# Kernel optimization log

Hardware: AMD Instinct MI355X
Metric: run time of the kernel (lower is better)

The kernel has to match this reference:

```python
import jax, jax.numpy as jnp
import numpy as np


def setup_inputs() -> dict:
    key = jax.random.key(0)
    k1, k2, k3, k4 = jax.random.split(key, 4)
    b, c, h, w = 16, 1024, 32, 32
    dim = h * w  # 1024
    x = jax.random.normal(k1, (b, c, h, w), dtype=jnp.float32)
    cond_img = jax.random.normal(k2, (b, c, h, w), dtype=jnp.float32)
    # torch nn.Linear weights: (out_features, in_features), y = x @ W.T
    Wq = jax.random.normal(k3, (dim, dim), dtype=jnp.float32) * (dim ** -0.5)
    Wkv = jax.random.normal(k4, (2 * dim, dim), dtype=jnp.float32) * (dim ** -0.5)
    return {"x": x, "cond_img": cond_img, "Wq": Wq, "Wkv": Wkv}


def reference(x, cond_img, Wq, Wkv):
    b, c, h, w = x.shape
    dim = h * w
    scale = dim ** -0.5
    xf = x.reshape(b, c, dim)          # (b, c, dim)
    cf = cond_img.reshape(b, c, dim)   # (b, c, dim)
    q = jnp.einsum('bcd,od->bco', xf, Wq)          # (b, c, dim)
    kv = jnp.einsum('bcd,od->bco', cf, Wkv)        # (b, c, 2*dim)
    k, v = jnp.split(kv, 2, axis=-1)               # each (b, c, dim)
    attn = jnp.einsum('bic,bjc->bij', q, k) * scale  # (b, c, c)
    attn = jax.nn.softmax(attn, axis=-1)
    out = jnp.einsum('bij,bjc->bic', attn, v)      # (b, c, dim)
    return out.reshape(b, c, h, w)
```

## Files before the change

### kernel.cpp

```cpp
#include <hip/hip_runtime.h>
#include <stdint.h>


typedef __bf16 bf16_t;
typedef bf16_t bf16x8 __attribute__((ext_vector_type(8)));
typedef float f32x4 __attribute__((ext_vector_type(4)));

#define AS1 __attribute__((address_space(1)))
#define AS3 __attribute__((address_space(3)))

__device__ __forceinline__ uint16_t f2bf(float f) {
  bf16_t h = (bf16_t)f;
  return __builtin_bit_cast(uint16_t, h);
}

__global__ __launch_bounds__(256) void cvt_all(
    const float* __restrict__ x, const float* __restrict__ c,
    const float* __restrict__ wq, const float* __restrict__ wkv,
    uint16_t* __restrict__ XB, uint16_t* __restrict__ CB,
    uint16_t* __restrict__ WQB, uint16_t* __restrict__ WKVB) {
  long i = (long)blockIdx.x * 256 + threadIdx.x;
  if (i >= 9175040) return;
  const float* src;
  uint16_t* dst;
  long off;
  if (i < 4194304) { src = x; dst = XB; off = i; }
  else if (i < 8388608) { src = c; dst = CB; off = i - 4194304; }
  else if (i < 8650752) { src = wq; dst = WQB; off = i - 8388608; }
  else { src = wkv; dst = WKVB; off = i - 8650752; }
  float4 v = ((const float4*)src)[off];
  ushort4 o;
  o.x = f2bf(v.x); o.y = f2bf(v.y); o.z = f2bf(v.z); o.w = f2bf(v.w);
  ((ushort4*)dst)[off] = o;
}

__device__ __forceinline__ void stage_tile(const uint16_t* __restrict__ g,
                                           int ldK, uint16_t* lds, int tid) {
#pragma unroll
  for (int i = 0; i < 4; ++i) {
    int cix = i * 512 + tid;
    int row = cix >> 3;
    int ch = cix & 7;
    int sch = ch ^ (row & 7);
    const uint16_t* gp = g + row * ldK + sch * 8;
    __builtin_amdgcn_global_load_lds((AS1 void*)gp,
                                     (AS3 void*)((uint8_t*)lds + cix * 16), 16,
                                     0, 0);
  }
}

template <int MODE>
__global__ __launch_bounds__(512, 2) void gemm_bt(
    const uint16_t* __restrict__ A, const uint16_t* __restrict__ B,
    void* __restrict__ C0, void* __restrict__ C1, int K, int N,
    long long sA, long long sB, long long sC, float scale) {
  __shared__ uint16_t smem[65536];

  const int tid = threadIdx.x;
  const int lane = tid & 63;
  const int wid = tid >> 6;
  const int wr = wid >> 2;
  const int wc = wid & 3;
  const int lr = lane & 15, lg = lane >> 4;
  const int ch0 = lr & 7;

  const int gx = gridDim.x, gy = gridDim.y;
  const int nwg = gx * gy * gridDim.z;
  int fid = blockIdx.x + gx * (blockIdx.y + gy * blockIdx.z);
  int swz = (fid & 7) * (nwg >> 3) + (fid >> 3);
  const int bx = swz % gx;
  const int rem = swz / gx;
  const int by = rem % gy;
  const int bz = rem / gy;

  const int row0 = by * 256;
  const int col0 = bx * 256;
  const uint16_t* At = A + (long long)bz * sA + (long long)row0 * K;
  const uint16_t* Bt = B + (long long)bz * sB + (long long)col0 * K;

  const int NT = K >> 6;

  stage_tile(At, K, smem, tid);
  stage_tile(Bt, K, smem + 32768, tid);
  stage_tile(At + 64, K, smem + 16384, tid);
  stage_tile(Bt + 64, K, smem + 49152, tid);
  asm volatile("s_waitcnt vmcnt(8)" ::: "memory");
  __builtin_amdgcn_s_barrier();

  f32x4 acc[8][4] = {};
  bf16x8 aA_[4][2];
  bf16x8 aB_[4][2];
  bf16x8 bF[4][2];

  {
    const uint8_t* sa = (const uint8_t*)smem;
#pragma unroll
    for (int mi = 0; mi < 4; ++mi)
#pragma unroll
      for (int kk = 0; kk < 2; ++kk)
        aA_[mi][kk] = *(const bf16x8*)(sa + (wr * 128 + mi * 16 + lr) * 128 +
                                       (((kk * 4 + lg) ^ ch0) << 4));
  }

  for (int t = 0; t < NT; ++t) {
    const uint8_t* sa = (const uint8_t*)(smem + (t & 1) * 16384);
    const uint8_t* sb = (const uint8_t*)(smem + 32768 + (t & 1) * 16384);

#pragma unroll
    for (int nj = 0; nj < 4; ++nj)
#pragma unroll
      for (int kk = 0; kk < 2; ++kk)
        bF[nj][kk] =
            *(const bf16x8*)(sb + (wc * 64 + nj * 16 + lr) * 128 +
                             (((kk * 4 + lg) ^ ch0) << 4));
#pragma unroll
    for (int mi = 0; mi < 4; ++mi)
#pragma unroll
      for (int kk = 0; kk < 2; ++kk)
        aB_[mi][kk] =
            *(const bf16x8*)(sa + (wr * 128 + 64 + mi * 16 + lr) * 128 +
                             (((kk * 4 + lg) ^ ch0) << 4));
    __builtin_amdgcn_s_setprio(1);
#pragma unroll
    for (int kk = 0; kk < 2; ++kk)
#pragma unroll
      for (int mi = 0; mi < 4; ++mi)
#pragma unroll
        for (int nj = 0; nj < 4; ++nj)
          acc[mi][nj] = __builtin_amdgcn_mfma_f32_16x16x32_bf16(
              aA_[mi][kk], bF[nj][kk], acc[mi][nj], 0, 0, 0);
    __builtin_amdgcn_s_setprio(0);
    if (t + 1 < NT) asm volatile("s_waitcnt vmcnt(4)" ::: "memory");
    asm volatile("s_waitcnt lgkmcnt(0)" ::: "memory");
    __builtin_amdgcn_s_barrier();

    if (t + 2 < NT) {
      stage_tile(At + (t + 2) * 64, K, smem + (t & 1) * 16384, tid);
      stage_tile(Bt + (t + 2) * 64, K, smem + 32768 + (t & 1) * 16384, tid);
    }
    if (t + 1 < NT) {
      const uint8_t* sa2 = (const uint8_t*)(smem + ((t + 1) & 1) * 16384);
#pragma unroll
      for (int mi = 0; mi < 4; ++mi)
#pragma unroll
        for (int kk = 0; kk < 2; ++kk)
          aA_[mi][kk] =
              *(const bf16x8*)(sa2 + (wr * 128 + mi * 16 + lr) * 128 +
                               (((kk * 4 + lg) ^ ch0) << 4));
    }
    __builtin_amdgcn_s_setprio(1);
#pragma unroll
    for (int kk = 0; kk < 2; ++kk)
#pragma unroll
      for (int mi = 0; mi < 4; ++mi)
#pragma unroll
        for (int nj = 0; nj < 4; ++nj)
          acc[4 + mi][nj] = __builtin_amdgcn_mfma_f32_16x16x32_bf16(
              aB_[mi][kk], bF[nj][kk], acc[4 + mi][nj], 0, 0, 0);
    __builtin_amdgcn_s_setprio(0);
    if (t + 2 < NT)
      asm volatile("s_waitcnt vmcnt(8)" ::: "memory");
    else
      asm volatile("s_waitcnt vmcnt(0)" ::: "memory");
    __builtin_amdgcn_s_barrier();
  }

  if (MODE == 1 && col0 >= 1024) {
    __syncthreads();
#pragma unroll
    for (int mi = 0; mi < 8; ++mi) {
#pragma unroll
      for (int ni = 0; ni < 4; ++ni) {
        const int cc = wc * 64 + ni * 16 + lr;
        const int jjb = wr * 128 + mi * 16 + lg * 4;
        ushort4 o;
        o.x = f2bf(acc[mi][ni][0]);
        o.y = f2bf(acc[mi][ni][1]);
        o.z = f2bf(acc[mi][ni][2]);
        o.w = f2bf(acc[mi][ni][3]);
        *(ushort4*)&smem[cc * 256 + (jjb ^ ((cc & 7) << 3))] = o;
      }
    }
    __syncthreads();
    const int b = row0 >> 10, jj0 = row0 & 1023;
    uint16_t* Vp = (uint16_t*)C1;
#pragma unroll
    for (int k = 0; k < 16; ++k) {
      const int cc = k * 16 + (tid >> 5);
      const int jb = (tid & 31) * 8;
      bf16x8 v = *(const bf16x8*)&smem[cc * 256 + (jb ^ ((cc & 7) << 3))];
      *(bf16x8*)(Vp + (long long)b * 1048576 +
                 (long long)(col0 - 1024 + cc) * 1024 + jj0 + jb) = v;
    }
    return;
  }
#pragma unroll
  for (int mi = 0; mi < 8; ++mi) {
#pragma unroll
    for (int ni = 0; ni < 4; ++ni) {
      const int row = row0 + wr * 128 + mi * 16 + lg * 4;
      const int col = col0 + wc * 64 + ni * 16 + lr;
      if (MODE == 0 || MODE == 1) {
        uint16_t* C = (uint16_t*)C0;
#pragma unroll
        for (int j = 0; j < 4; ++j)
          C[(long long)(row + j) * (MODE == 1 ? 1024 : N) + col] =
              f2bf(acc[mi][ni][j]);
      } else {
        float* C = (float*)C0;
#pragma unroll
        for (int j = 0; j < 4; ++j)
          C[(long long)bz * sC + (long long)(row + j) * N + col] =
              acc[mi][ni][j] * scale;
      }
    }
  }
}

__global__ __launch_bounds__(256) void softmax_rows(const float* __restrict__ S,
                                                    uint16_t* __restrict__ P) {
  const int row = blockIdx.x;
  const int t = threadIdx.x;
  const int w = t >> 6, l = t & 63;
  __shared__ float red[8];

  const float4 v = ((const float4*)(S + (long long)row * 1024))[t];
  float m = fmaxf(fmaxf(v.x, v.y), fmaxf(v.z, v.w));
#pragma unroll
  for (int o = 1; o < 64; o <<= 1) m = fmaxf(m, __shfl_xor(m, o, 64));
  if (l == 0) red[w] = m;
  __syncthreads();
  m = fmaxf(fmaxf(red[0], red[1]), fmaxf(red[2], red[3]));

  float e0 = __expf(v.x - m), e1 = __expf(v.y - m);
  float e2 = __expf(v.z - m), e3 = __expf(v.w - m);
  float s = e0 + e1 + e2 + e3;
#pragma unroll
  for (int o = 1; o < 64; o <<= 1) s += __shfl_xor(s, o, 64);
  if (l == 0) red[4 + w] = s;
  __syncthreads();
  s = red[4] + red[5] + red[6] + red[7];
  const float inv = 1.0f / s;

  ushort4 o4;
  o4.x = f2bf(e0 * inv); o4.y = f2bf(e1 * inv);
  o4.z = f2bf(e2 * inv); o4.w = f2bf(e3 * inv);
  ((ushort4*)P)[(long long)row * 256 + t] = o4;
}

extern "C" void kernel_launch(void* const* d_in, const int* in_sizes, int n_in,
                              void* d_out, int out_size, void* d_ws, size_t ws_size,
                              hipStream_t stream) {
  const float* x    = (const float*)d_in[0];
  const float* cond = (const float*)d_in[1];
  const float* Wq   = (const float*)d_in[2];
  const float* Wkv  = (const float*)d_in[3];
  float* out = (float*)d_out;

  uint8_t* ws = (uint8_t*)d_ws;
  const long long MiB = 1ll << 20;
  uint16_t* XB   = (uint16_t*)(ws + 0 * MiB);
  uint16_t* CB   = (uint16_t*)(ws + 32 * MiB);
  float*    S    = (float*)(ws + 0 * MiB);
  uint16_t* WQB  = (uint16_t*)(ws + 64 * MiB);
  uint16_t* WKVB = (uint16_t*)(ws + 66 * MiB);
  uint16_t* Q    = (uint16_t*)(ws + 70 * MiB);
  uint16_t* Kb   = (uint16_t*)(ws + 102 * MiB);
  uint16_t* VT   = (uint16_t*)(ws + 134 * MiB);

  cvt_all<<<35840, 256, 0, stream>>>(x, cond, Wq, Wkv, XB, CB, WQB, WKVB);

  gemm_bt<0><<<dim3(4, 64, 1), 512, 0, stream>>>(XB, WQB, Q, nullptr, 1024,
                                                 1024, 0, 0, 0, 1.0f);
  gemm_bt<1><<<dim3(8, 64, 1), 512, 0, stream>>>(CB, WKVB, Kb, VT, 1024, 2048,
                                                 0, 0, 0, 1.0f);
  gemm_bt<2><<<dim3(4, 4, 16), 512, 0, stream>>>(Q, Kb, S, nullptr, 1024, 1024,
                                                 1048576, 1048576, 1048576,
                                                 0.03125f);
  softmax_rows<<<16384, 256, 0, stream>>>(S, Q);
  gemm_bt<2><<<dim3(4, 4, 16), 512, 0, stream>>>(Q, VT, out, nullptr, 1024,
                                                 1024, 1048576, 1048576,
                                                 1048576, 1.0f);
}
```

Before: 239.7 us.

## Fuse fp32-to-bf16 activation conversion into projection GEMM A-tile loading

The separate conversion pass for x and cond_img is removed. The Q and KV projection GEMMs now read fp32 A tiles straight into registers, convert them to bf16, and write them into swizzled LDS, with the register prefetch running one tile ahead. Only the weights are still converted by a small kernel. This drops a full read and write of the activations, at the cost of register staging, more VGPR pressure, and hand-tuned vmcnt waits that may hurt overlap.

```diff
diff --git a/kernel.cpp b/kernel.cpp
--- a/kernel.cpp
+++ b/kernel.cpp
@@ -14,20 +14,16 @@
   return __builtin_bit_cast(uint16_t, h);
 }
 
-__global__ __launch_bounds__(256) void cvt_all(
-    const float* __restrict__ x, const float* __restrict__ c,
-    const float* __restrict__ wq, const float* __restrict__ wkv,
-    uint16_t* __restrict__ XB, uint16_t* __restrict__ CB,
-    uint16_t* __restrict__ WQB, uint16_t* __restrict__ WKVB) {
-  long i = (long)blockIdx.x * 256 + threadIdx.x;
-  if (i >= 9175040) return;
+__global__ __launch_bounds__(256) void cvt_w(const float* __restrict__ wq,
+                                             const float* __restrict__ wkv,
+                                             uint16_t* __restrict__ WQB,
+                                             uint16_t* __restrict__ WKVB) {
+  int i = blockIdx.x * 256 + threadIdx.x;
   const float* src;
   uint16_t* dst;
-  long off;
-  if (i < 4194304) { src = x; dst = XB; off = i; }
-  else if (i < 8388608) { src = c; dst = CB; off = i - 4194304; }
-  else if (i < 8650752) { src = wq; dst = WQB; off = i - 8388608; }
-  else { src = wkv; dst = WKVB; off = i - 8650752; }
+  int off;
+  if (i < 262144) { src = wq; dst = WQB; off = i; }
+  else { src = wkv; dst = WKVB; off = i - 262144; }
   float4 v = ((const float4*)src)[off];
   ushort4 o;
   o.x = f2bf(v.x); o.y = f2bf(v.y); o.z = f2bf(v.z); o.w = f2bf(v.w);
@@ -49,9 +45,28 @@
   }
 }
 
-template <int MODE>
+#define ISSUE_A(TOFF)                                                       \
+  _Pragma("unroll") for (int kq = 0; kq < 4; ++kq) {                        \
+    int j = kq * 512 + tid;                                                 \
+    const float* gp = At32 + (long long)(j >> 3) * K + (TOFF) + (j & 7) * 8;\
+    areg[kq][0] = *(const f32x4*)gp;                                        \
+    areg[kq][1] = *(const f32x4*)(gp + 4);                                  \
+  }
+#define WRITE_A(BUF)                                                        \
+  _Pragma("unroll") for (int kq = 0; kq < 4; ++kq) {                        \
+    int j = kq * 512 + tid;                                                 \
+    int row = j >> 3, ch = j & 7;                                           \
+    bf16x8 o;                                                               \
+    o[0] = (bf16_t)areg[kq][0][0]; o[1] = (bf16_t)areg[kq][0][1];           \
+    o[2] = (bf16_t)areg[kq][0][2]; o[3] = (bf16_t)areg[kq][0][3];           \
+    o[4] = (bf16_t)areg[kq][1][0]; o[5] = (bf16_t)areg[kq][1][1];           \
+    o[6] = (bf16_t)areg[kq][1][2]; o[7] = (bf16_t)areg[kq][1][3];           \
+    *(bf16x8*)((uint8_t*)(BUF) + row * 128 + ((ch ^ (row & 7)) << 4)) = o;  \
+  }
+
+template <int MODE, bool AFP32>
 __global__ __launch_bounds__(512, 2) void gemm_bt(
-    const uint16_t* __restrict__ A, const uint16_t* __restrict__ B,
+    const void* __restrict__ Araw, const uint16_t* __restrict__ B,
     void* __restrict__ C0, void* __restrict__ C1, int K, int N,
     long long sA, long long sB, long long sC, float scale) {
   __shared__ uint16_t smem[65536];
@@ -75,17 +90,36 @@
 
   const int row0 = by * 256;
   const int col0 = bx * 256;
-  const uint16_t* At = A + (long long)bz * sA + (long long)row0 * K;
+  const float* At32 = nullptr;
+  const uint16_t* At16 = nullptr;
+  if constexpr (AFP32)
+    At32 = (const float*)Araw + (long long)bz * sA + (long long)row0 * K;
+  else
+    At16 = (const uint16_t*)Araw + (long long)bz * sA + (long long)row0 * K;
   const uint16_t* Bt = B + (long long)bz * sB + (long long)col0 * K;
 
   const int NT = K >> 6;
 
-  stage_tile(At, K, smem, tid);
-  stage_tile(Bt, K, smem + 32768, tid);
-  stage_tile(At + 64, K, smem + 16384, tid);
-  stage_tile(Bt + 64, K, smem + 49152, tid);
-  asm volatile("s_waitcnt vmcnt(8)" ::: "memory");
-  __builtin_amdgcn_s_barrier();
+  f32x4 areg[4][2];
+
+  if constexpr (AFP32) {
+    stage_tile(Bt, K, smem + 32768, tid);
+    stage_tile(Bt + 64, K, smem + 49152, tid);
+    ISSUE_A(0);
+    WRITE_A(smem);
+    ISSUE_A(64);
+    WRITE_A(smem + 16384);
+    if (NT > 2) ISSUE_A(128);
+    asm volatile("s_waitcnt vmcnt(8) lgkmcnt(0)" ::: "memory");
+    __builtin_amdgcn_s_barrier();
+  } else {
+    stage_tile(At16, K, smem, tid);
+    stage_tile(Bt, K, smem + 32768, tid);
+    stage_tile(At16 + 64, K, smem + 16384, tid);
+    stage_tile(Bt + 64, K, smem + 49152, tid);
+    asm volatile("s_waitcnt vmcnt(8)" ::: "memory");
+    __builtin_amdgcn_s_barrier();
+  }
 
   f32x4 acc[8][4] = {};
   bf16x8 aA_[4][2];
@@ -110,16 +144,14 @@
     for (int nj = 0; nj < 4; ++nj)
 #pragma unroll
       for (int kk = 0; kk < 2; ++kk)
-        bF[nj][kk] =
-            *(const bf16x8*)(sb + (wc * 64 + nj * 16 + lr) * 128 +
-                             (((kk * 4 + lg) ^ ch0) << 4));
+        bF[nj][kk] = *(const bf16x8*)(sb + (wc * 64 + nj * 16 + lr) * 128 +
+                                      (((kk * 4 + lg) ^ ch0) << 4));
 #pragma unroll
     for (int mi = 0; mi < 4; ++mi)
 #pragma unroll
       for (int kk = 0; kk < 2; ++kk)
-        aB_[mi][kk] =
-            *(const bf16x8*)(sa + (wr * 128 + 64 + mi * 16 + lr) * 128 +
-                             (((kk * 4 + lg) ^ ch0) << 4));
+        aB_[mi][kk] = *(const bf16x8*)(sa + (wr * 128 + 64 + mi * 16 + lr) * 128 +
+                                       (((kk * 4 + lg) ^ ch0) << 4));
     __builtin_amdgcn_s_setprio(1);
 #pragma unroll
     for (int kk = 0; kk < 2; ++kk)
@@ -130,13 +162,22 @@
           acc[mi][nj] = __builtin_amdgcn_mfma_f32_16x16x32_bf16(
               aA_[mi][kk], bF[nj][kk], acc[mi][nj], 0, 0, 0);
     __builtin_amdgcn_s_setprio(0);
-    if (t + 1 < NT) asm volatile("s_waitcnt vmcnt(4)" ::: "memory");
+    if constexpr (!AFP32) {
+      if (t + 1 < NT) asm volatile("s_waitcnt vmcnt(4)" ::: "memory");
+    }
     asm volatile("s_waitcnt lgkmcnt(0)" ::: "memory");
     __builtin_amdgcn_s_barrier();
 
-    if (t + 2 < NT) {
-      stage_tile(At + (t + 2) * 64, K, smem + (t & 1) * 16384, tid);
-      stage_tile(Bt + (t + 2) * 64, K, smem + 32768 + (t & 1) * 16384, tid);
+    if constexpr (AFP32) {
+      if (t + 2 < NT) WRITE_A(smem + (t & 1) * 16384);
+      if (t + 3 < NT) ISSUE_A((t + 3) * 64);
+      if (t + 2 < NT)
+        stage_tile(Bt + (t + 2) * 64, K, smem + 32768 + (t & 1) * 16384, tid);
+    } else {
+      if (t + 2 < NT) {
+        stage_tile(At16 + (t + 2) * 64, K, smem + (t & 1) * 16384, tid);
+        stage_tile(Bt + (t + 2) * 64, K, smem + 32768 + (t & 1) * 16384, tid);
+      }
     }
     if (t + 1 < NT) {
       const uint8_t* sa2 = (const uint8_t*)(smem + ((t + 1) & 1) * 16384);
@@ -144,9 +185,8 @@
       for (int mi = 0; mi < 4; ++mi)
 #pragma unroll
         for (int kk = 0; kk < 2; ++kk)
-          aA_[mi][kk] =
-              *(const bf16x8*)(sa2 + (wr * 128 + mi * 16 + lr) * 128 +
-                               (((kk * 4 + lg) ^ ch0) << 4));
+          aA_[mi][kk] = *(const bf16x8*)(sa2 + (wr * 128 + mi * 16 + lr) * 128 +
+                                         (((kk * 4 + lg) ^ ch0) << 4));
     }
     __builtin_amdgcn_s_setprio(1);
 #pragma unroll
@@ -158,10 +198,19 @@
           acc[4 + mi][nj] = __builtin_amdgcn_mfma_f32_16x16x32_bf16(
               aB_[mi][kk], bF[nj][kk], acc[4 + mi][nj], 0, 0, 0);
     __builtin_amdgcn_s_setprio(0);
-    if (t + 2 < NT)
-      asm volatile("s_waitcnt vmcnt(8)" ::: "memory");
-    else
-      asm volatile("s_waitcnt vmcnt(0)" ::: "memory");
+    if constexpr (AFP32) {
+      if (t + 3 < NT)
+        asm volatile("s_waitcnt vmcnt(12)" ::: "memory");
+      else if (t + 2 < NT)
+        asm volatile("s_waitcnt vmcnt(4)" ::: "memory");
+      else if (t + 1 < NT)
+        asm volatile("s_waitcnt vmcnt(0)" ::: "memory");
+    } else {
+      if (t + 2 < NT)
+        asm volatile("s_waitcnt vmcnt(8)" ::: "memory");
+      else
+        asm volatile("s_waitcnt vmcnt(0)" ::: "memory");
+    }
     __builtin_amdgcn_s_barrier();
   }
 
@@ -259,26 +308,22 @@
 
   uint8_t* ws = (uint8_t*)d_ws;
   const long long MiB = 1ll << 20;
-  uint16_t* XB   = (uint16_t*)(ws + 0 * MiB);
-  uint16_t* CB   = (uint16_t*)(ws + 32 * MiB);
-  float*    S    = (float*)(ws + 0 * MiB);
-  uint16_t* WQB  = (uint16_t*)(ws + 64 * MiB);
-  uint16_t* WKVB = (uint16_t*)(ws + 66 * MiB);
-  uint16_t* Q    = (uint16_t*)(ws + 70 * MiB);
-  uint16_t* Kb   = (uint16_t*)(ws + 102 * MiB);
-  uint16_t* VT   = (uint16_t*)(ws + 134 * MiB);
-
-  cvt_all<<<35840, 256, 0, stream>>>(x, cond, Wq, Wkv, XB, CB, WQB, WKVB);
-
-  gemm_bt<0><<<dim3(4, 64, 1), 512, 0, stream>>>(XB, WQB, Q, nullptr, 1024,
-                                                 1024, 0, 0, 0, 1.0f);
-  gemm_bt<1><<<dim3(8, 64, 1), 512, 0, stream>>>(CB, WKVB, Kb, VT, 1024, 2048,
-                                                 0, 0, 0, 1.0f);
-  gemm_bt<2><<<dim3(4, 4, 16), 512, 0, stream>>>(Q, Kb, S, nullptr, 1024, 1024,
-                                                 1048576, 1048576, 1048576,
-                                                 0.03125f);
+  uint16_t* Q    = (uint16_t*)(ws + 0 * MiB);
+  uint16_t* Kb   = (uint16_t*)(ws + 32 * MiB);
+  uint16_t* VT   = (uint16_t*)(ws + 64 * MiB);
+  float*    S    = (float*)(ws + 96 * MiB);
+  uint16_t* WQB  = (uint16_t*)(ws + 160 * MiB);
+  uint16_t* WKVB = (uint16_t*)(ws + 162 * MiB);
+
+  cvt_w<<<3072, 256, 0, stream>>>(Wq, Wkv, WQB, WKVB);
+
+  gemm_bt<0, true><<<dim3(4, 64, 1), 512, 0, stream>>>(
+      x, WQB, Q, nullptr, 1024, 1024, 0, 0, 0, 1.0f);
+  gemm_bt<1, true><<<dim3(8, 64, 1), 512, 0, stream>>>(
+      cond, WKVB, Kb, VT, 1024, 2048, 0, 0, 0, 1.0f);
+  gemm_bt<2, false><<<dim3(4, 4, 16), 512, 0, stream>>>(
+      Q, Kb, S, nullptr, 1024, 1024, 1048576, 1048576, 1048576, 0.03125f);
   softmax_rows<<<16384, 256, 0, stream>>>(S, Q);
-  gemm_bt<2><<<dim3(4, 4, 16), 512, 0, stream>>>(Q, VT, out, nullptr, 1024,
-                                                 1024, 1048576, 1048576,
-                                                 1048576, 1.0f);
-}
+  gemm_bt<2, false><<<dim3(4, 4, 16), 512, 0, stream>>>(
+      Q, VT, out, nullptr, 1024, 1024, 1048576, 1048576, 1048576, 1.0f);
+}
```

Result: slower. 662.9 us (+176.6%).
